# Kernel optimization log

Hardware: AMD Instinct MI355X
Metric: run time of the kernel (lower is better)

## Reference

```python
import jax, jax.numpy as jnp
import numpy as np

L = 3          # num_gc_layers
DIM = 128      # hidden dim (== num_features)
BN_EPS = 1e-5


def _bn(h, gamma, beta):
    # torch BatchNorm1d training-mode normalization (biased variance)
    m = h.mean(axis=0)
    v = h.var(axis=0)
    return gamma * (h - m) * jax.lax.rsqrt(v + BN_EPS) + beta


def setup_inputs() -> dict:
    key = jax.random.key(0)
    ks = jax.random.split(key, 24)
    N, E, G = 50000, 600000, 256
    s = 0.05
    inp = {
        "x": jax.random.normal(ks[0], (N, DIM), jnp.float32),
        "src": jax.random.randint(ks[1], (E,), 0, N, jnp.int32),
        "dst": jax.random.randint(ks[2], (E,), 0, N, jnp.int32),
        "batch": jnp.sort(jax.random.randint(ks[3], (N,), 0, G, jnp.int32)),
        "n_graphs": G,
        # GIN MLP params (stacked over layers; num_features == dim)
        "conv_w1": jax.random.normal(ks[4], (L, DIM, DIM), jnp.float32) * s,
        "conv_b1": jnp.zeros((L, DIM), jnp.float32),
        "conv_w2": jax.random.normal(ks[5], (L, DIM, DIM), jnp.float32) * s,
        "conv_b2": jnp.zeros((L, DIM), jnp.float32),
        "bn_gamma": jnp.ones((L, DIM), jnp.float32),
        "bn_beta": jnp.zeros((L, DIM), jnp.float32),
        # summary weighter (dim -> 1)
        "sw_w": jax.random.normal(ks[6], (DIM, 1), jnp.float32) * s,
        "sw_b": jnp.zeros((1,), jnp.float32),
        # VAE heads
        "nmu_w": jax.random.normal(ks[7], (DIM, DIM), jnp.float32) * s,
        "nmu_b": jnp.zeros((DIM,), jnp.float32),
        "nlv_w": jax.random.normal(ks[8], (DIM, DIM), jnp.float32) * s,
        "nlv_b": jnp.zeros((DIM,), jnp.float32),
        "gmu_w": jax.random.normal(ks[9], (DIM, DIM), jnp.float32) * s,
        "gmu_b": jnp.zeros((DIM,), jnp.float32),
        "glv_w": jax.random.normal(ks[10], (DIM, DIM), jnp.float32) * s,
        "glv_b": jnp.zeros((DIM,), jnp.float32),
        # head BN params, order: [node_mu, node_logvar, graph_mu, graph_logvar]
        "head_gamma": jnp.ones((4, DIM), jnp.float32),
        "head_beta": jnp.zeros((4, DIM), jnp.float32),
    }
    return inp


def reference(x, src, dst, batch, n_graphs,
              conv_w1, conv_b1, conv_w2, conv_b2, bn_gamma, bn_beta,
              sw_w, sw_b, nmu_w, nmu_b, nlv_w, nlv_b,
              gmu_w, gmu_b, glv_w, glv_b, head_gamma, head_beta):
    N = x.shape[0]
    for i in range(L):
        # GINConv (eps=0): h = nn(x + sum_{j->i} x_j)
        agg = jax.ops.segment_sum(x[src], dst, num_segments=N)  # [N, dim]
        h = x + agg
        h = jax.nn.relu(h @ conv_w1[i] + conv_b1[i]) @ conv_w2[i] + conv_b2[i]
        x = _bn(jax.nn.relu(h), bn_gamma[i], bn_beta[i])

    w = jax.nn.sigmoid(x @ sw_w + sw_b)           # [N, 1]
    summary_info = w * x                          # [N, dim]
    noisy_info = (1.0 - w) * x                    # [N, dim]
    slots = jax.ops.segment_sum(summary_info, batch, num_segments=n_graphs)  # [G, dim]

    node_mu = _bn(jax.nn.relu(noisy_info @ nmu_w + nmu_b), head_gamma[0], head_beta[0])
    node_logvar = _bn(jax.nn.relu(noisy_info @ nlv_w + nlv_b), head_gamma[1], head_beta[1])
    graph_mu = _bn(jax.nn.relu(slots @ gmu_w + gmu_b), head_gamma[2], head_beta[2])
    graph_logvar = _bn(jax.nn.relu(slots @ glv_w + glv_b), head_gamma[3], head_beta[3])
    return (node_mu, node_logvar, graph_mu, graph_logvar)
```

## Files before the change

kernel.cpp:

```cpp
#include <hip/hip_runtime.h>
#include <hip/hip_bf16.h>

#define DIM 128
#define BN_EPS 1e-5f
#define NSTRIPE 32

typedef unsigned short ushortT;
typedef __attribute__((ext_vector_type(8))) short short8;
typedef __attribute__((ext_vector_type(4))) float floatx4;

__device__ __forceinline__ float bflo(unsigned u) { return __uint_as_float(u << 16); }
__device__ __forceinline__ float bfhi(unsigned u) { return __uint_as_float(u & 0xffff0000u); }
__device__ __forceinline__ float bf2f(ushortT h) { return __uint_as_float(((unsigned)h) << 16); }
__device__ __forceinline__ ushortT f2bf(float f) {
    unsigned x = __float_as_uint(f);
    unsigned r = (x + 0x7fff + ((x >> 16) & 1)) >> 16;
    return (ushortT)r;
}
__device__ __forceinline__ void decode8(const unsigned* ap, short8& hi, short8& lo) {
#pragma unroll
    for (int j = 0; j < 8; ++j) {
        hi[j] = (short)(ap[j] >> 16);
        lo[j] = (short)(ap[j] & 0xffffu);
    }
}
__device__ __forceinline__ void acc8(float* a, uint4 v) {
    a[0] += bflo(v.x); a[1] += bfhi(v.x);
    a[2] += bflo(v.y); a[3] += bfhi(v.y);
    a[4] += bflo(v.z); a[5] += bfhi(v.z);
    a[6] += bflo(v.w); a[7] += bfhi(v.w);
}

__global__ __launch_bounds__(256) void hist_kernel(
    const int* __restrict__ dst, int* __restrict__ deg, int E)
{
    int e = blockIdx.x * 256 + threadIdx.x;
    if (e < E) atomicAdd(&deg[dst[e]], 1);
}

__global__ __launch_bounds__(256) void scan1_kernel(
    const int* __restrict__ deg, int* __restrict__ iscan,
    int* __restrict__ bsum, int N)
{
    __shared__ int s[256];
    int t = threadIdx.x;
    int i = blockIdx.x * 256 + t;
    int v = (i < N) ? deg[i] : 0;
    s[t] = v;
    __syncthreads();
#pragma unroll
    for (int off = 1; off < 256; off <<= 1) {
        int u = (t >= off) ? s[t - off] : 0;
        __syncthreads();
        s[t] += u;
        __syncthreads();
    }
    if (i < N) iscan[i] = s[t];
    if (t == 255) bsum[blockIdx.x] = s[255];
}

__global__ __launch_bounds__(256) void scan2_kernel(int* __restrict__ bsum, int nb)
{
    __shared__ int s[256];
    int t = threadIdx.x;
    int v = (t < nb) ? bsum[t] : 0;
    s[t] = v;
    __syncthreads();
#pragma unroll
    for (int off = 1; off < 256; off <<= 1) {
        int u = (t >= off) ? s[t - off] : 0;
        __syncthreads();
        s[t] += u;
        __syncthreads();
    }
    if (t < nb) bsum[t] = s[t] - v;
}

__global__ __launch_bounds__(256) void scan3_kernel(
    const int* __restrict__ iscan, const int* __restrict__ bsum,
    const int* __restrict__ deg, int* __restrict__ row_ptr,
    int* __restrict__ cur, int N)
{
    int i = blockIdx.x * 256 + threadIdx.x;
    if (i < N) {
        int inc = iscan[i] + bsum[i >> 8];
        row_ptr[i + 1] = inc;
        cur[i] = inc - deg[i];
    }
    if (i == 0) row_ptr[0] = 0;
}

__global__ __launch_bounds__(256) void fill_kernel(
    const int* __restrict__ src, const int* __restrict__ dst,
    int* __restrict__ cur, int* __restrict__ eidx, int E)
{
    int e = blockIdx.x * 256 + threadIdx.x;
    if (e < E) {
        int pos = atomicAdd(&cur[dst[e]], 1);
        eidx[pos] = src[e];
    }
}

__global__ __launch_bounds__(256) void convw_kernel(
    const float* __restrict__ cw1, const float* __restrict__ cw2,
    const float* __restrict__ nmu, const float* __restrict__ nlv,
    const float* __restrict__ gmu, const float* __restrict__ glv,
    ushortT* __restrict__ whi, ushortT* __restrict__ wlo)
{
    int tid = blockIdx.x * 256 + threadIdx.x;
    int mat = tid >> 14;
    int i   = tid & 16383;
    int n = i >> 7, k = i & 127;
    const float* Wm = (mat < 3) ? cw1 + (size_t)mat * 16384
                    : (mat < 6) ? cw2 + (size_t)(mat - 3) * 16384
                    : (mat == 6) ? nmu : (mat == 7) ? nlv
                    : (mat == 8) ? gmu : glv;
    float w = Wm[k * DIM + n];
    ushortT h = f2bf(w);
    whi[(size_t)mat * 16384 + i] = h;
    wlo[(size_t)mat * 16384 + i] = f2bf(w - bf2f(h));
}

__global__ __launch_bounds__(256) void convx_kernel(
    const float* __restrict__ x, ushortT* __restrict__ xb, int n8)
{
    int i = blockIdx.x * 256 + threadIdx.x;
    if (i >= n8) return;
    const float4* xp = (const float4*)x;
    float4 a = xp[2 * i], b = xp[2 * i + 1];
    uint4 o;
    o.x = (unsigned)f2bf(a.x) | ((unsigned)f2bf(a.y) << 16);
    o.y = (unsigned)f2bf(a.z) | ((unsigned)f2bf(a.w) << 16);
    o.z = (unsigned)f2bf(b.x) | ((unsigned)f2bf(b.y) << 16);
    o.w = (unsigned)f2bf(b.z) | ((unsigned)f2bf(b.w) << 16);
    ((uint4*)xb)[i] = o;
}

__global__ __launch_bounds__(256) void merge_stats_kernel(
    const float* __restrict__ sbuf, float* __restrict__ out)
{
    int t = threadIdx.x;
    float s = 0.f;
#pragma unroll
    for (int i = 0; i < NSTRIPE; ++i) s += sbuf[i * 256 + t];
    out[t] = s;
}

__global__ __launch_bounds__(256) void layer_fused_kernel(
    const ushortT* __restrict__ Xb, const int* __restrict__ row_ptr,
    const int* __restrict__ eidx,
    const float* __restrict__ ssum, const float* __restrict__ ssq,
    const float* __restrict__ gamma, const float* __restrict__ beta,
    const ushortT* __restrict__ W1hi, const ushortT* __restrict__ W1lo,
    const float* __restrict__ b1,
    const ushortT* __restrict__ W2hi, const ushortT* __restrict__ W2lo,
    const float* __restrict__ b2,
    ushortT* __restrict__ rout, float* __restrict__ sdst,
    int M, float invM)
{
    __shared__ unsigned As[32][DIM + 4];
    __shared__ float ls[DIM], lsq[DIM];
    int t = threadIdx.x;
    int wave = t >> 6, lane = t & 63, quad = lane >> 4, l16 = lane & 15;
    int m0 = blockIdx.x * 32;

    {
        int nloc = t >> 3;
        int c0   = (t & 7) * 16;
        int node = m0 + nloc;
        float acc[16];
#pragma unroll
        for (int j = 0; j < 16; ++j) acc[j] = 0.f;
        if (node < M) {
            int b = row_ptr[node];
            int e = row_ptr[node + 1];
            const ushortT* xrow = Xb + (size_t)node * DIM + c0;
            acc8(&acc[0], *(const uint4*)(xrow));
            acc8(&acc[8], *(const uint4*)(xrow + 8));
            int i = b;
            for (; i + 4 <= e; i += 4) {
                int s0 = eidx[i], s1 = eidx[i + 1], s2 = eidx[i + 2], s3 = eidx[i + 3];
                const ushortT* p0 = Xb + (size_t)s0 * DIM + c0;
                const ushortT* p1 = Xb + (size_t)s1 * DIM + c0;
                const ushortT* p2 = Xb + (size_t)s2 * DIM + c0;
                const ushortT* p3 = Xb + (size_t)s3 * DIM + c0;
                uint4 v00 = *(const uint4*)(p0), v01 = *(const uint4*)(p0 + 8);
                uint4 v10 = *(const uint4*)(p1), v11 = *(const uint4*)(p1 + 8);
                uint4 v20 = *(const uint4*)(p2), v21 = *(const uint4*)(p2 + 8);
                uint4 v30 = *(const uint4*)(p3), v31 = *(const uint4*)(p3 + 8);
                acc8(&acc[0], v00); acc8(&acc[8], v01);
                acc8(&acc[0], v10); acc8(&acc[8], v11);
                acc8(&acc[0], v20); acc8(&acc[8], v21);
                acc8(&acc[0], v30); acc8(&acc[8], v31);
            }
            for (; i < e; ++i) {
                const ushortT* sp = Xb + (size_t)eidx[i] * DIM + c0;
                acc8(&acc[0], *(const uint4*)(sp));
                acc8(&acc[8], *(const uint4*)(sp + 8));
            }
            if (ssum) {
                float cnt = (float)(e - b + 1);
#pragma unroll
                for (int jq = 0; jq < 4; ++jq) {
                    int c = c0 + jq * 4;
                    float4 sm = *(const float4*)(ssum + c);
                    float4 sq = *(const float4*)(ssq + c);
                    float4 gm = *(const float4*)(gamma + c);
                    float4 bt = *(const float4*)(beta + c);
                    float m, sc;
                    m = sm.x * invM; sc = gm.x * rsqrtf(sq.x * invM - m * m + BN_EPS);
                    acc[jq * 4 + 0] = sc * acc[jq * 4 + 0] + cnt * (bt.x - sc * m);
                    m = sm.y * invM; sc = gm.y * rsqrtf(sq.y * invM - m * m + BN_EPS);
                    acc[jq * 4 + 1] = sc * acc[jq * 4 + 1] + cnt * (bt.y - sc * m);
                    m = sm.z * invM; sc = gm.z * rsqrtf(sq.z * invM - m * m + BN_EPS);
                    acc[jq * 4 + 2] = sc * acc[jq * 4 + 2] + cnt * (bt.z - sc * m);
                    m = sm.w * invM; sc = gm.w * rsqrtf(sq.w * invM - m * m + BN_EPS);
                    acc[jq * 4 + 3] = sc * acc[jq * 4 + 3] + cnt * (bt.w - sc * m);
                }
            }
        }
        unsigned pk[16];
#pragma unroll
        for (int j = 0; j < 16; ++j) {
            ushortT h = f2bf(acc[j]);
            ushortT l = f2bf(acc[j] - bf2f(h));
            pk[j] = ((unsigned)h << 16) | l;
        }
#pragma unroll
        for (int j4 = 0; j4 < 4; ++j4)
            *(uint4*)&As[nloc][c0 + j4 * 4] = *(uint4*)&pk[j4 * 4];
    }
    if (t < DIM) { ls[t] = 0.f; lsq[t] = 0.f; }
    __syncthreads();

    int cbase = wave * 32;
    floatx4 acc[2][2];
#pragma unroll
    for (int mt = 0; mt < 2; ++mt)
#pragma unroll
        for (int nt = 0; nt < 2; ++nt)
            acc[mt][nt] = (floatx4){0.f, 0.f, 0.f, 0.f};

#pragma unroll
    for (int ks = 0; ks < 4; ++ks) {
        int k0 = ks * 32 + quad * 8;
        short8 bhi[2], blo[2];
#pragma unroll
        for (int nt = 0; nt < 2; ++nt) {
            const size_t woff = (size_t)(cbase + nt * 16 + l16) * DIM + k0;
            bhi[nt] = *(const short8*)(W1hi + woff);
            blo[nt] = *(const short8*)(W1lo + woff);
        }
#pragma unroll
        for (int mt = 0; mt < 2; ++mt) {
            int lr = mt * 16 + l16;
            unsigned ap[8];
            *(uint4*)&ap[0] = *(const uint4*)&As[lr][k0];
            *(uint4*)&ap[4] = *(const uint4*)&As[lr][k0 + 4];
            short8 ahi, alo;
            decode8(ap, ahi, alo);
#pragma unroll
            for (int nt = 0; nt < 2; ++nt) {
                acc[mt][nt] = __builtin_amdgcn_mfma_f32_16x16x32_bf16(ahi, bhi[nt], acc[mt][nt], 0, 0, 0);
                acc[mt][nt] = __builtin_amdgcn_mfma_f32_16x16x32_bf16(alo, bhi[nt], acc[mt][nt], 0, 0, 0);
                acc[mt][nt] = __builtin_amdgcn_mfma_f32_16x16x32_bf16(ahi, blo[nt], acc[mt][nt], 0, 0, 0);
            }
        }
    }
    __syncthreads();

#pragma unroll
    for (int nt = 0; nt < 2; ++nt) {
        int col = cbase + nt * 16 + l16;
        float bcol = b1[col];
#pragma unroll
        for (int mt = 0; mt < 2; ++mt)
#pragma unroll
            for (int r = 0; r < 4; ++r) {
                int lr = mt * 16 + quad * 4 + r;
                float v = fmaxf(acc[mt][nt][r] + bcol, 0.f);
                ushortT hv = f2bf(v);
                ushortT lv = f2bf(v - bf2f(hv));
                As[lr][col] = ((unsigned)hv << 16) | lv;
            }
    }
    __syncthreads();

#pragma unroll
    for (int mt = 0; mt < 2; ++mt)
#pragma unroll
        for (int nt = 0; nt < 2; ++nt)
            acc[mt][nt] = (floatx4){0.f, 0.f, 0.f, 0.f};

#pragma unroll
    for (int ks = 0; ks < 4; ++ks) {
        int k0 = ks * 32 + quad * 8;
        short8 bhi[2], blo[2];
#pragma unroll
        for (int nt = 0; nt < 2; ++nt) {
            const size_t woff = (size_t)(cbase + nt * 16 + l16) * DIM + k0;
            bhi[nt] = *(const short8*)(W2hi + woff);
            blo[nt] = *(const short8*)(W2lo + woff);
        }
#pragma unroll
        for (int mt = 0; mt < 2; ++mt) {
            int lr = mt * 16 + l16;
            unsigned ap[8];
            *(uint4*)&ap[0] = *(const uint4*)&As[lr][k0];
            *(uint4*)&ap[4] = *(const uint4*)&As[lr][k0 + 4];
            short8 ahi, alo;
            decode8(ap, ahi, alo);
#pragma unroll
            for (int nt = 0; nt < 2; ++nt) {
                acc[mt][nt] = __builtin_amdgcn_mfma_f32_16x16x32_bf16(ahi, bhi[nt], acc[mt][nt], 0, 0, 0);
                acc[mt][nt] = __builtin_amdgcn_mfma_f32_16x16x32_bf16(alo, bhi[nt], acc[mt][nt], 0, 0, 0);
                acc[mt][nt] = __builtin_amdgcn_mfma_f32_16x16x32_bf16(ahi, blo[nt], acc[mt][nt], 0, 0, 0);
            }
        }
    }
#pragma unroll
    for (int nt = 0; nt < 2; ++nt) {
        int col = cbase + nt * 16 + l16;
        float bcol = b2[col];
        float s = 0.f, sq = 0.f;
#pragma unroll
        for (int mt = 0; mt < 2; ++mt)
#pragma unroll
            for (int r = 0; r < 4; ++r) {
                int gr = m0 + mt * 16 + quad * 4 + r;
                if (gr < M) {
                    float v = fmaxf(acc[mt][nt][r] + bcol, 0.f);
                    rout[(size_t)gr * DIM + col] = f2bf(v);
                    s += v;
                    sq += v * v;
                }
            }
        s  += __shfl_xor(s, 16);  s  += __shfl_xor(s, 32);
        sq += __shfl_xor(sq, 16); sq += __shfl_xor(sq, 32);
        if (quad == 0) {
            atomicAdd(&ls[col], s);
            atomicAdd(&lsq[col], sq);
        }
    }
    __syncthreads();
    float* dstp = sdst + (size_t)(blockIdx.x & (NSTRIPE - 1)) * 256;
    if (t < 128) atomicAdd(&dstp[t], ls[t]);
    else         atomicAdd(&dstp[t], lsq[t - 128]);
}

__global__ __launch_bounds__(256) void heads_kernel(
    const unsigned* __restrict__ AP,
    const ushortT* __restrict__ WAhi, const ushortT* __restrict__ WAlo,
    const float* __restrict__ bA, ushortT* __restrict__ hA, float* __restrict__ sdstA,
    const ushortT* __restrict__ WBhi, const ushortT* __restrict__ WBlo,
    const float* __restrict__ bB, ushortT* __restrict__ hB, float* __restrict__ sdstB,
    int M)
{
    __shared__ float lsA[DIM], lsqA[DIM], lsB[DIM], lsqB[DIM];
    int t = threadIdx.x;
    int wave = t >> 6, lane = t & 63, quad = lane >> 4, l16 = lane & 15;
    int m0 = blockIdx.x * 64;
    int cbase = wave * 32;

    if (t < DIM) { lsA[t] = 0.f; lsqA[t] = 0.f; lsB[t] = 0.f; lsqB[t] = 0.f; }
    __syncthreads();

    floatx4 accA[4][2], accB[4][2];
#pragma unroll
    for (int mt = 0; mt < 4; ++mt)
#pragma unroll
        for (int nt = 0; nt < 2; ++nt) {
            accA[mt][nt] = (floatx4){0.f, 0.f, 0.f, 0.f};
            accB[mt][nt] = (floatx4){0.f, 0.f, 0.f, 0.f};
        }

    for (int ks = 0; ks < 4; ++ks) {
        int k0 = ks * 32 + quad * 8;
        short8 bAhi[2], bAlo[2], bBhi[2], bBlo[2];
#pragma unroll
        for (int nt = 0; nt < 2; ++nt) {
            const size_t woff = (size_t)(cbase + nt * 16 + l16) * DIM + k0;
            bAhi[nt] = *(const short8*)(WAhi + woff);
            bAlo[nt] = *(const short8*)(WAlo + woff);
            bBhi[nt] = *(const short8*)(WBhi + woff);
            bBlo[nt] = *(const short8*)(WBlo + woff);
        }
#pragma unroll
        for (int mt = 0; mt < 4; ++mt) {
            int row = m0 + mt * 16 + l16;
            unsigned ap[8] = {0, 0, 0, 0, 0, 0, 0, 0};
            if (row < M) {
                *(uint4*)&ap[0] = *(const uint4*)(AP + (size_t)row * DIM + k0);
                *(uint4*)&ap[4] = *(const uint4*)(AP + (size_t)row * DIM + k0 + 4);
            }
            short8 ahi, alo;
            decode8(ap, ahi, alo);
#pragma unroll
            for (int nt = 0; nt < 2; ++nt) {
                accA[mt][nt] = __builtin_amdgcn_mfma_f32_16x16x32_bf16(ahi, bAhi[nt], accA[mt][nt], 0, 0, 0);
                accA[mt][nt] = __builtin_amdgcn_mfma_f32_16x16x32_bf16(alo, bAhi[nt], accA[mt][nt], 0, 0, 0);
                accA[mt][nt] = __builtin_amdgcn_mfma_f32_16x16x32_bf16(ahi, bAlo[nt], accA[mt][nt], 0, 0, 0);
                accB[mt][nt] = __builtin_amdgcn_mfma_f32_16x16x32_bf16(ahi, bBhi[nt], accB[mt][nt], 0, 0, 0);
                accB[mt][nt] = __builtin_amdgcn_mfma_f32_16x16x32_bf16(alo, bBhi[nt], accB[mt][nt], 0, 0, 0);
                accB[mt][nt] = __builtin_amdgcn_mfma_f32_16x16x32_bf16(ahi, bBlo[nt], accB[mt][nt], 0, 0, 0);
            }
        }
    }

#pragma unroll
    for (int nt = 0; nt < 2; ++nt) {
        int col = cbase + nt * 16 + l16;
        float bcA = bA[col], bcB = bB[col];
        float sA = 0.f, sqA = 0.f, sB = 0.f, sqB = 0.f;
#pragma unroll
        for (int mt = 0; mt < 4; ++mt)
#pragma unroll
            for (int r = 0; r < 4; ++r) {
                int gr = m0 + mt * 16 + quad * 4 + r;
                if (gr < M) {
                    size_t off = (size_t)gr * DIM + col;
                    float vA = fmaxf(accA[mt][nt][r] + bcA, 0.f);
                    float vB = fmaxf(accB[mt][nt][r] + bcB, 0.f);
                    hA[off] = f2bf(vA);
                    hB[off] = f2bf(vB);
                    sA += vA; sqA += vA * vA;
                    sB += vB; sqB += vB * vB;
                }
            }
        sA += __shfl_xor(sA, 16);  sA += __shfl_xor(sA, 32);
        sqA += __shfl_xor(sqA, 16); sqA += __shfl_xor(sqA, 32);
        sB += __shfl_xor(sB, 16);  sB += __shfl_xor(sB, 32);
        sqB += __shfl_xor(sqB, 16); sqB += __shfl_xor(sqB, 32);
        if (quad == 0) {
            atomicAdd(&lsA[col], sA);
            atomicAdd(&lsqA[col], sqA);
            atomicAdd(&lsB[col], sB);
            atomicAdd(&lsqB[col], sqB);
        }
    }
    __syncthreads();
    int stripe = blockIdx.x & (NSTRIPE - 1);
    float* dA = sdstA + (size_t)stripe * 256;
    float* dB = sdstB + (size_t)stripe * 256;
    if (t < 128) { atomicAdd(&dA[t], lsA[t]); atomicAdd(&dB[t], lsB[t]); }
    else         { atomicAdd(&dA[t], lsqA[t - 128]); atomicAdd(&dB[t], lsqB[t - 128]); }
}

__global__ __launch_bounds__(256) void gemm_graph_kernel(
    const float* __restrict__ A32,
    const ushortT* __restrict__ Whi, const ushortT* __restrict__ Wlo,
    const float* __restrict__ bias, float* __restrict__ C,
    float* __restrict__ ssum, float* __restrict__ ssq, int M)
{
    __shared__ float ls[DIM], lsq[DIM];
    int t     = threadIdx.x;
    int wave  = t >> 6;
    int lane  = t & 63;
    int quad  = lane >> 4;
    int l16   = lane & 15;
    int m0    = blockIdx.x * 64;
    int cbase = wave * 32;

    if (t < DIM) { ls[t] = 0.f; lsq[t] = 0.f; }
    __syncthreads();

    floatx4 acc[4][2];
#pragma unroll
    for (int mt = 0; mt < 4; ++mt)
#pragma unroll
        for (int nt = 0; nt < 2; ++nt)
            acc[mt][nt] = (floatx4){0.f, 0.f, 0.f, 0.f};

    for (int ks = 0; ks < 4; ++ks) {
        int k0 = ks * 32 + quad * 8;
        short8 bhi[2], blo[2];
#pragma unroll
        for (int nt = 0; nt < 2; ++nt) {
            const size_t woff = (size_t)(cbase + nt * 16 + l16) * DIM + k0;
            bhi[nt] = *(const short8*)(Whi + woff);
            blo[nt] = *(const short8*)(Wlo + woff);
        }
#pragma unroll
        for (int mt = 0; mt < 4; ++mt) {
            int row = m0 + mt * 16 + l16;
            short8 ahi = {0,0,0,0,0,0,0,0};
            short8 alo = {0,0,0,0,0,0,0,0};
            if (row < M) {
                float av[8];
                *(float4*)&av[0] = *(const float4*)(A32 + (size_t)row * DIM + k0);
                *(float4*)&av[4] = *(const float4*)(A32 + (size_t)row * DIM + k0 + 4);
#pragma unroll
                for (int j = 0; j < 8; ++j) {
                    ushortT hv = f2bf(av[j]);
                    ahi[j] = (short)hv;
                    alo[j] = (short)f2bf(av[j] - bf2f(hv));
                }
            }
#pragma unroll
            for (int nt = 0; nt < 2; ++nt) {
                acc[mt][nt] = __builtin_amdgcn_mfma_f32_16x16x32_bf16(ahi, bhi[nt], acc[mt][nt], 0, 0, 0);
                acc[mt][nt] = __builtin_amdgcn_mfma_f32_16x16x32_bf16(alo, bhi[nt], acc[mt][nt], 0, 0, 0);
                acc[mt][nt] = __builtin_amdgcn_mfma_f32_16x16x32_bf16(ahi, blo[nt], acc[mt][nt], 0, 0, 0);
            }
        }
    }

#pragma unroll
    for (int nt = 0; nt < 2; ++nt) {
        int col = cbase + nt * 16 + l16;
        float bcol = bias[col];
        float s = 0.f, sq = 0.f;
#pragma unroll
        for (int mt = 0; mt < 4; ++mt)
#pragma unroll
            for (int r = 0; r < 4; ++r) {
                int gr = m0 + mt * 16 + quad * 4 + r;
                if (gr < M) {
                    float v = fmaxf(acc[mt][nt][r] + bcol, 0.f);
                    C[(size_t)gr * DIM + col] = v;
                    s += v;
                    sq += v * v;
                }
            }
        s  += __shfl_xor(s, 16);  s  += __shfl_xor(s, 32);
        sq += __shfl_xor(sq, 16); sq += __shfl_xor(sq, 32);
        if (quad == 0) {
            atomicAdd(&ls[col], s);
            atomicAdd(&lsq[col], sq);
        }
    }
    __syncthreads();
    if (t < DIM) {
        atomicAdd(&ssum[t], ls[t]);
        atomicAdd(&ssq[t], lsq[t]);
    }
}

__global__ __launch_bounds__(256) void bn_apply_kernel(
    const float* __restrict__ R, float* __restrict__ O,
    const float* __restrict__ sums, const float* __restrict__ sqsums,
    const float* __restrict__ gamma, const float* __restrict__ beta, int M)
{
    int idx = blockIdx.x * 256 + threadIdx.x;
    if (idx >= M * 32) return;
    int c4 = idx & 31;
    float invM = 1.0f / (float)M;
    float4 v = ((const float4*)R)[idx];
    float o[4] = {v.x, v.y, v.z, v.w};
#pragma unroll
    for (int j = 0; j < 4; ++j) {
        int c = c4 * 4 + j;
        float m   = sums[c] * invM;
        float var = sqsums[c] * invM - m * m;
        float sc  = gamma[c] * rsqrtf(var + BN_EPS);
        o[j] = sc * (o[j] - m) + beta[c];
    }
    ((float4*)O)[idx] = make_float4(o[0], o[1], o[2], o[3]);
}

__global__ __launch_bounds__(256) void bn_apply_bf16_kernel(
    const ushortT* __restrict__ R, float* __restrict__ O,
    const float* __restrict__ sums, const float* __restrict__ sqsums,
    const float* __restrict__ gamma, const float* __restrict__ beta, int M)
{
    int idx = blockIdx.x * 256 + threadIdx.x;
    if (idx >= M * 32) return;
    int c4 = idx & 31;
    float invM = 1.0f / (float)M;
    uint2 u = ((const uint2*)R)[idx];
    float o[4] = {bflo(u.x), bfhi(u.x), bflo(u.y), bfhi(u.y)};
#pragma unroll
    for (int j = 0; j < 4; ++j) {
        int c = c4 * 4 + j;
        float m   = sums[c] * invM;
        float var = sqsums[c] * invM - m * m;
        float sc  = gamma[c] * rsqrtf(var + BN_EPS);
        o[j] = sc * (o[j] - m) + beta[c];
    }
    ((float4*)O)[idx] = make_float4(o[0], o[1], o[2], o[3]);
}

__global__ __launch_bounds__(256) void weigh_split_kernel(
    const ushortT* __restrict__ R, const int* __restrict__ batch,
    const float* __restrict__ ssum, const float* __restrict__ ssq,
    const float* __restrict__ gamma, const float* __restrict__ beta,
    const float* __restrict__ sw_w, const float* __restrict__ sw_b,
    unsigned* __restrict__ noisyP, float* __restrict__ slots, int N, float invM)
{
    __shared__ float part[256];
    __shared__ float wsh[128];
    int t  = threadIdx.x;
    int r0 = blockIdx.x * 128;

    {
        int row  = r0 + (t >> 1);
        int cs   = (t & 1) * 64;
        float d = 0.f;
        if (row < N) {
            for (int c = cs; c < cs + 64; c += 4) {
                uint2 u = *(const uint2*)(R + (size_t)row * DIM + c);
                float rv[4] = {bflo(u.x), bfhi(u.x), bflo(u.y), bfhi(u.y)};
                float4 sm = *(const float4*)(ssum + c);
                float4 sq = *(const float4*)(ssq + c);
                float4 gm = *(const float4*)(gamma + c);
                float4 bt = *(const float4*)(beta + c);
                float4 sw = *(const float4*)(sw_w + c);
                float m, sc;
                m = sm.x * invM; sc = gm.x * rsqrtf(sq.x * invM - m * m + BN_EPS);
                d += (sc * (rv[0] - m) + bt.x) * sw.x;
                m = sm.y * invM; sc = gm.y * rsqrtf(sq.y * invM - m * m + BN_EPS);
                d += (sc * (rv[1] - m) + bt.y) * sw.y;
                m = sm.z * invM; sc = gm.z * rsqrtf(sq.z * invM - m * m + BN_EPS);
                d += (sc * (rv[2] - m) + bt.z) * sw.z;
                m = sm.w * invM; sc = gm.w * rsqrtf(sq.w * invM - m * m + BN_EPS);
                d += (sc * (rv[3] - m) + bt.w) * sw.w;
            }
        }
        part[t] = d;
    }
    __syncthreads();
    if (t < 128) {
        float dd = part[2 * t] + part[2 * t + 1];
        wsh[t] = 1.0f / (1.0f + expf(-(dd + sw_b[0])));
    }
    __syncthreads();

    int c    = t & 127;
    int half = t >> 7;
    int rend = r0 + 128;
    if (rend > N) rend = N;
    float m   = ssum[c] * invM;
    float var = ssq[c] * invM - m * m;
    float sc  = gamma[c] * rsqrtf(var + BN_EPS);
    float sh  = beta[c] - sc * m;
    int curg = -1;
    float acc = 0.f;
    for (int r = r0 + half; r < rend; r += 2) {
        float xv = sc * bf2f(R[(size_t)r * DIM + c]) + sh;
        float w  = wsh[r - r0];
        float nv = (1.f - w) * xv;
        ushortT hv = f2bf(nv);
        ushortT lv = f2bf(nv - bf2f(hv));
        noisyP[(size_t)r * DIM + c] = ((unsigned)hv << 16) | lv;
        int g = batch[r];
        if (g != curg) {
            if (curg >= 0) atomicAdd(&slots[(size_t)curg * DIM + c], acc);
            curg = g;
            acc = 0.f;
        }
        acc += w * xv;
    }
    if (curg >= 0) atomicAdd(&slots[(size_t)curg * DIM + c], acc);
}

extern "C" void kernel_launch(void* const* d_in, const int* in_sizes, int n_in,
                              void* d_out, int out_size, void* d_ws, size_t ws_size,
                              hipStream_t stream)
{
    const float* x      = (const float*)d_in[0];
    const int*   src    = (const int*)d_in[1];
    const int*   dst    = (const int*)d_in[2];
    const int*   batch  = (const int*)d_in[3];
    const float* cw1    = (const float*)d_in[5];
    const float* cb1    = (const float*)d_in[6];
    const float* cw2    = (const float*)d_in[7];
    const float* cb2    = (const float*)d_in[8];
    const float* bng    = (const float*)d_in[9];
    const float* bnb    = (const float*)d_in[10];
    const float* sw_w   = (const float*)d_in[11];
    const float* sw_b   = (const float*)d_in[12];
    const float* nmu_w  = (const float*)d_in[13];
    const float* nmu_b  = (const float*)d_in[14];
    const float* nlv_w  = (const float*)d_in[15];
    const float* nlv_b  = (const float*)d_in[16];
    const float* gmu_w  = (const float*)d_in[17];
    const float* gmu_b  = (const float*)d_in[18];
    const float* glv_w  = (const float*)d_in[19];
    const float* glv_b  = (const float*)d_in[20];
    const float* hgam   = (const float*)d_in[21];
    const float* hbet   = (const float*)d_in[22];

    const int N = in_sizes[0] / DIM;
    const int E = in_sizes[1];
    const int G = (out_size / DIM - 2 * N) / 2;

    float* out0 = (float*)d_out;
    float* out1 = out0 + (size_t)N * DIM;
    float* out2 = out1 + (size_t)N * DIM;
    float* out3 = out2 + (size_t)G * DIM;

    char* wp = (char*)d_ws;
    auto alloc = [&](size_t bytes) {
        char* p = wp;
        wp += (bytes + 255) & ~(size_t)255;
        return p;
    };
    ushortT*  xbf   = (ushortT*)alloc((size_t)N * DIM * 2);
    ushortT*  rA    = (ushortT*)alloc((size_t)N * DIM * 2);
    ushortT*  rB    = (ushortT*)alloc((size_t)N * DIM * 2);
    unsigned* noisyP= (unsigned*)alloc((size_t)N * DIM * 4);
    ushortT*  whi   = (ushortT*)alloc((size_t)10 * 16384 * 2);
    ushortT*  wlo   = (ushortT*)alloc((size_t)10 * 16384 * 2);
    float* slots    = (float*)alloc((size_t)G * DIM * 4);
    float* stats    = (float*)alloc((size_t)7 * 256 * 4);
    float* sbuf     = (float*)alloc((size_t)5 * NSTRIPE * 256 * 4);
    int* row_ptr    = (int*)alloc((size_t)(N + 2) * 4);
    int* eidx       = (int*)alloc((size_t)E * 4);
    int* deg   = (int*)noisyP;
    int* iscan = deg + N;
    int* bsum  = iscan + N;
    int* cur   = bsum + 256;

    auto SS = [&](int i) { return stats + (size_t)i * 256; };
    auto SQ = [&](int i) { return stats + (size_t)i * 256 + 128; };
    auto SB = [&](int i) { return sbuf + (size_t)i * NSTRIPE * 256; };

    const int edge_blocks  = (E + 255) / 256;
    const int scan_blocks  = (N + 255) / 256;
    const int layer_blocks = (N + 31) / 32;
    const int heads_blocks = (N + 63) / 64;
    const int g16_blocks   = (N * 16 + 255) / 256;
    const int g32_blocks   = (N * 32 + 255) / 256;
    const float invN = 1.0f / (float)N;

    hipMemsetAsync(stats, 0, (size_t)7 * 256 * 4, stream);
    hipMemsetAsync(sbuf, 0, (size_t)5 * NSTRIPE * 256 * 4, stream);
    hipMemsetAsync(slots, 0, (size_t)G * DIM * 4, stream);
    hipMemsetAsync(deg, 0, (size_t)N * 4, stream);

    convw_kernel<<<(10 * 16384) / 256, 256, 0, stream>>>(
        cw1, cw2, nmu_w, nlv_w, gmu_w, glv_w, whi, wlo);
    convx_kernel<<<g16_blocks, 256, 0, stream>>>(x, xbf, N * 16);

    hist_kernel<<<edge_blocks, 256, 0, stream>>>(dst, deg, E);
    scan1_kernel<<<scan_blocks, 256, 0, stream>>>(deg, iscan, bsum, N);
    scan2_kernel<<<1, 256, 0, stream>>>(bsum, scan_blocks);
    scan3_kernel<<<scan_blocks, 256, 0, stream>>>(iscan, bsum, deg, row_ptr, cur, N);
    fill_kernel<<<edge_blocks, 256, 0, stream>>>(src, dst, cur, eidx, E);

    const ushortT* lin[3]  = {xbf, rA, rB};
    ushortT*       lout[3] = {rA, rB, rA};
    for (int l = 0; l < 3; ++l) {
        const float* sums_prev = (l == 0) ? nullptr : SS(l - 1);
        const float* sq_prev   = (l == 0) ? nullptr : SQ(l - 1);
        const float* g_prev    = (l == 0) ? nullptr : bng + (size_t)(l - 1) * DIM;
        const float* b_prev    = (l == 0) ? nullptr : bnb + (size_t)(l - 1) * DIM;
        layer_fused_kernel<<<layer_blocks, 256, 0, stream>>>(
            lin[l], row_ptr, eidx,
            sums_prev, sq_prev, g_prev, b_prev,
            whi + (size_t)l * 16384, wlo + (size_t)l * 16384, cb1 + (size_t)l * DIM,
            whi + (size_t)(3 + l) * 16384, wlo + (size_t)(3 + l) * 16384, cb2 + (size_t)l * DIM,
            lout[l], SB(l), N, invN);
        merge_stats_kernel<<<1, 256, 0, stream>>>(SB(l), SS(l));
    }
    ushortT* rfin = rA;
    ushortT* hA   = rB;
    ushortT* hB   = xbf;

    weigh_split_kernel<<<(N + 127) / 128, 256, 0, stream>>>(
        rfin, batch, SS(2), SQ(2), bng + 2 * DIM, bnb + 2 * DIM,
        sw_w, sw_b, noisyP, slots, N, invN);

    heads_kernel<<<heads_blocks, 256, 0, stream>>>(
        noisyP,
        whi + (size_t)6 * 16384, wlo + (size_t)6 * 16384, nmu_b, hA, SB(3),
        whi + (size_t)7 * 16384, wlo + (size_t)7 * 16384, nlv_b, hB, SB(4), N);
    merge_stats_kernel<<<1, 256, 0, stream>>>(SB(3), SS(3));
    merge_stats_kernel<<<1, 256, 0, stream>>>(SB(4), SS(4));
    bn_apply_bf16_kernel<<<g32_blocks, 256, 0, stream>>>(
        hA, out0, SS(3), SQ(3), hgam + 0 * DIM, hbet + 0 * DIM, N);
    bn_apply_bf16_kernel<<<g32_blocks, 256, 0, stream>>>(
        hB, out1, SS(4), SQ(4), hgam + 1 * DIM, hbet + 1 * DIM, N);

    const int gemm_blocks_G = (G + 63) / 64;
    gemm_graph_kernel<<<gemm_blocks_G, 256, 0, stream>>>(
        slots, whi + (size_t)8 * 16384, wlo + (size_t)8 * 16384,
        gmu_b, out2, SS(5), SQ(5), G);
    gemm_graph_kernel<<<gemm_blocks_G, 256, 0, stream>>>(
        slots, whi + (size_t)9 * 16384, wlo + (size_t)9 * 16384,
        glv_b, out3, SS(6), SQ(6), G);
    bn_apply_kernel<<<(G * 32 + 255) / 256, 256, 0, stream>>>(
        out2, out2, SS(5), SQ(5), hgam + 2 * DIM, hbet + 2 * DIM, G);
    bn_apply_kernel<<<(G * 32 + 255) / 256, 256, 0, stream>>>(
        out3, out3, SS(6), SQ(6), hgam + 3 * DIM, hbet + 3 * DIM, G);
}
```

Measured before the change: 509.4 us.

## Merge small launches, fold stat merging into consumers, deepen gather unroll

Folds the weight conversion, input bf16 conversion and all memsets into a single prep kernel. Each layer kernel and the weigh-split kernel now reduces the striped statistics buffer itself instead of relying on separate merge launches. Paired head GEMM and BN-apply launches are combined into dual-dispatch kernels. The neighbour gather gains an 8-way unrolled loop, and the layer kernel gets a launch-bounds occupancy hint. The aim is to cut launch count and latency in exchange for redundant per-block stripe reduction work and higher register pressure.

```diff
diff --git a/kernel.cpp b/kernel.cpp
--- a/kernel.cpp
+++ b/kernel.cpp
@@ -101,55 +101,57 @@
     }
 }
 
-__global__ __launch_bounds__(256) void convw_kernel(
+__global__ __launch_bounds__(256) void prep_kernel(
     const float* __restrict__ cw1, const float* __restrict__ cw2,
     const float* __restrict__ nmu, const float* __restrict__ nlv,
     const float* __restrict__ gmu, const float* __restrict__ glv,
-    ushortT* __restrict__ whi, ushortT* __restrict__ wlo)
-{
-    int tid = blockIdx.x * 256 + threadIdx.x;
-    int mat = tid >> 14;
-    int i   = tid & 16383;
-    int n = i >> 7, k = i & 127;
-    const float* Wm = (mat < 3) ? cw1 + (size_t)mat * 16384
-                    : (mat < 6) ? cw2 + (size_t)(mat - 3) * 16384
-                    : (mat == 6) ? nmu : (mat == 7) ? nlv
-                    : (mat == 8) ? gmu : glv;
-    float w = Wm[k * DIM + n];
-    ushortT h = f2bf(w);
-    whi[(size_t)mat * 16384 + i] = h;
-    wlo[(size_t)mat * 16384 + i] = f2bf(w - bf2f(h));
-}
-
-__global__ __launch_bounds__(256) void convx_kernel(
-    const float* __restrict__ x, ushortT* __restrict__ xb, int n8)
-{
-    int i = blockIdx.x * 256 + threadIdx.x;
-    if (i >= n8) return;
-    const float4* xp = (const float4*)x;
-    float4 a = xp[2 * i], b = xp[2 * i + 1];
-    uint4 o;
-    o.x = (unsigned)f2bf(a.x) | ((unsigned)f2bf(a.y) << 16);
-    o.y = (unsigned)f2bf(a.z) | ((unsigned)f2bf(a.w) << 16);
-    o.z = (unsigned)f2bf(b.x) | ((unsigned)f2bf(b.y) << 16);
-    o.w = (unsigned)f2bf(b.z) | ((unsigned)f2bf(b.w) << 16);
-    ((uint4*)xb)[i] = o;
-}
-
-__global__ __launch_bounds__(256) void merge_stats_kernel(
-    const float* __restrict__ sbuf, float* __restrict__ out)
-{
-    int t = threadIdx.x;
-    float s = 0.f;
-#pragma unroll
-    for (int i = 0; i < NSTRIPE; ++i) s += sbuf[i * 256 + t];
-    out[t] = s;
-}
-
-__global__ __launch_bounds__(256) void layer_fused_kernel(
+    ushortT* __restrict__ whi, ushortT* __restrict__ wlo,
+    const float* __restrict__ x, ushortT* __restrict__ xb, int n8, int cxBlocks,
+    float4* __restrict__ zsbuf, int sbufQ,
+    float4* __restrict__ zslots, int slotsQ,
+    float4* __restrict__ zdeg, int degQ,
+    float4* __restrict__ zstats, int statsQ)
+{
+    int b = blockIdx.x, t = threadIdx.x;
+    if (b < 640) {
+        int tid = b * 256 + t;
+        int mat = tid >> 14;
+        int i   = tid & 16383;
+        int n = i >> 7, k = i & 127;
+        const float* Wm = (mat < 3) ? cw1 + (size_t)mat * 16384
+                        : (mat < 6) ? cw2 + (size_t)(mat - 3) * 16384
+                        : (mat == 6) ? nmu : (mat == 7) ? nlv
+                        : (mat == 8) ? gmu : glv;
+        float w = Wm[k * DIM + n];
+        ushortT h = f2bf(w);
+        whi[(size_t)mat * 16384 + i] = h;
+        wlo[(size_t)mat * 16384 + i] = f2bf(w - bf2f(h));
+    } else if (b < 640 + cxBlocks) {
+        int i = (b - 640) * 256 + t;
+        if (i < n8) {
+            const float4* xp = (const float4*)x;
+            float4 a = xp[2 * i], bb = xp[2 * i + 1];
+            uint4 o;
+            o.x = (unsigned)f2bf(a.x) | ((unsigned)f2bf(a.y) << 16);
+            o.y = (unsigned)f2bf(a.z) | ((unsigned)f2bf(a.w) << 16);
+            o.z = (unsigned)f2bf(bb.x) | ((unsigned)f2bf(bb.y) << 16);
+            o.w = (unsigned)f2bf(bb.z) | ((unsigned)f2bf(bb.w) << 16);
+            ((uint4*)xb)[i] = o;
+        }
+    } else {
+        int q = (b - 640 - cxBlocks) * 256 + t;
+        float4 z = make_float4(0.f, 0.f, 0.f, 0.f);
+        if (q < sbufQ) zsbuf[q] = z;
+        else if ((q -= sbufQ) < slotsQ) zslots[q] = z;
+        else if ((q -= slotsQ) < degQ) zdeg[q] = z;
+        else if ((q -= degQ) < statsQ) zstats[q] = z;
+    }
+}
+
+__global__ __launch_bounds__(256, 4) void layer_fused_kernel(
     const ushortT* __restrict__ Xb, const int* __restrict__ row_ptr,
     const int* __restrict__ eidx,
-    const float* __restrict__ ssum, const float* __restrict__ ssq,
+    const float* __restrict__ sprev,
     const float* __restrict__ gamma, const float* __restrict__ beta,
     const ushortT* __restrict__ W1hi, const ushortT* __restrict__ W1lo,
     const float* __restrict__ b1,
@@ -160,9 +162,19 @@
 {
     __shared__ unsigned As[32][DIM + 4];
     __shared__ float ls[DIM], lsq[DIM];
+    __shared__ float pstat[256];
     int t = threadIdx.x;
     int wave = t >> 6, lane = t & 63, quad = lane >> 4, l16 = lane & 15;
     int m0 = blockIdx.x * 32;
+
+    if (sprev) {
+        float s = 0.f;
+#pragma unroll
+        for (int i = 0; i < NSTRIPE; ++i) s += sprev[i * 256 + t];
+        pstat[t] = s;
+    }
+    if (t < DIM) { ls[t] = 0.f; lsq[t] = 0.f; }
+    __syncthreads();
 
     {
         int nloc = t >> 3;
@@ -178,6 +190,22 @@
             acc8(&acc[0], *(const uint4*)(xrow));
             acc8(&acc[8], *(const uint4*)(xrow + 8));
             int i = b;
+            for (; i + 8 <= e; i += 8) {
+                const ushortT* p[8];
+#pragma unroll
+                for (int j = 0; j < 8; ++j) p[j] = Xb + (size_t)eidx[i + j] * DIM + c0;
+                uint4 va[8], vb[8];
+#pragma unroll
+                for (int j = 0; j < 8; ++j) {
+                    va[j] = *(const uint4*)(p[j]);
+                    vb[j] = *(const uint4*)(p[j] + 8);
+                }
+#pragma unroll
+                for (int j = 0; j < 8; ++j) {
+                    acc8(&acc[0], va[j]);
+                    acc8(&acc[8], vb[j]);
+                }
+            }
             for (; i + 4 <= e; i += 4) {
                 int s0 = eidx[i], s1 = eidx[i + 1], s2 = eidx[i + 2], s3 = eidx[i + 3];
                 const ushortT* p0 = Xb + (size_t)s0 * DIM + c0;
@@ -198,13 +226,13 @@
                 acc8(&acc[0], *(const uint4*)(sp));
                 acc8(&acc[8], *(const uint4*)(sp + 8));
             }
-            if (ssum) {
+            if (sprev) {
                 float cnt = (float)(e - b + 1);
 #pragma unroll
                 for (int jq = 0; jq < 4; ++jq) {
                     int c = c0 + jq * 4;
-                    float4 sm = *(const float4*)(ssum + c);
-                    float4 sq = *(const float4*)(ssq + c);
+                    float4 sm = *(const float4*)&pstat[c];
+                    float4 sq = *(const float4*)&pstat[128 + c];
                     float4 gm = *(const float4*)(gamma + c);
                     float4 bt = *(const float4*)(beta + c);
                     float m, sc;
@@ -230,7 +258,6 @@
         for (int j4 = 0; j4 < 4; ++j4)
             *(uint4*)&As[nloc][c0 + j4 * 4] = *(uint4*)&pk[j4 * 4];
     }
-    if (t < DIM) { ls[t] = 0.f; lsq[t] = 0.f; }
     __syncthreads();
 
     int cbase = wave * 32;
@@ -446,19 +473,39 @@
     else         { atomicAdd(&dA[t], lsqA[t - 128]); atomicAdd(&dB[t], lsqB[t - 128]); }
 }
 
-__global__ __launch_bounds__(256) void gemm_graph_kernel(
+__global__ __launch_bounds__(256) void merge_stats2_kernel(
+    const float* __restrict__ sA, float* __restrict__ oA,
+    const float* __restrict__ sB, float* __restrict__ oB)
+{
+    const float* s = blockIdx.x ? sB : sA;
+    float* o = blockIdx.x ? oB : oA;
+    int t = threadIdx.x;
+    float v = 0.f;
+#pragma unroll
+    for (int i = 0; i < NSTRIPE; ++i) v += s[i * 256 + t];
+    o[t] = v;
+}
+
+__global__ __launch_bounds__(256) void gemm_graph_dual_kernel(
     const float* __restrict__ A32,
-    const ushortT* __restrict__ Whi, const ushortT* __restrict__ Wlo,
-    const float* __restrict__ bias, float* __restrict__ C,
-    float* __restrict__ ssum, float* __restrict__ ssq, int M)
+    const ushortT* __restrict__ W8hi, const ushortT* __restrict__ W8lo,
+    const float* __restrict__ b8, float* __restrict__ C8, float* __restrict__ st8,
+    const ushortT* __restrict__ W9hi, const ushortT* __restrict__ W9lo,
+    const float* __restrict__ b9, float* __restrict__ C9, float* __restrict__ st9,
+    int M, int nb)
 {
     __shared__ float ls[DIM], lsq[DIM];
+    int bb = blockIdx.x;
+    const ushortT* Whi; const ushortT* Wlo; const float* bias; float* C; float* st;
+    if (bb < nb) { Whi = W8hi; Wlo = W8lo; bias = b8; C = C8; st = st8; }
+    else { bb -= nb; Whi = W9hi; Wlo = W9lo; bias = b9; C = C9; st = st9; }
+
     int t     = threadIdx.x;
     int wave  = t >> 6;
     int lane  = t & 63;
     int quad  = lane >> 4;
     int l16   = lane & 15;
-    int m0    = blockIdx.x * 64;
+    int m0    = bb * 64;
     int cbase = wave * 32;
 
     if (t < DIM) { ls[t] = 0.f; lsq[t] = 0.f; }
@@ -531,39 +578,23 @@
     }
     __syncthreads();
     if (t < DIM) {
-        atomicAdd(&ssum[t], ls[t]);
-        atomicAdd(&ssq[t], lsq[t]);
-    }
-}
-
-__global__ __launch_bounds__(256) void bn_apply_kernel(
-    const float* __restrict__ R, float* __restrict__ O,
-    const float* __restrict__ sums, const float* __restrict__ sqsums,
-    const float* __restrict__ gamma, const float* __restrict__ beta, int M)
-{
-    int idx = blockIdx.x * 256 + threadIdx.x;
-    if (idx >= M * 32) return;
-    int c4 = idx & 31;
-    float invM = 1.0f / (float)M;
-    float4 v = ((const float4*)R)[idx];
-    float o[4] = {v.x, v.y, v.z, v.w};
-#pragma unroll
-    for (int j = 0; j < 4; ++j) {
-        int c = c4 * 4 + j;
-        float m   = sums[c] * invM;
-        float var = sqsums[c] * invM - m * m;
-        float sc  = gamma[c] * rsqrtf(var + BN_EPS);
-        o[j] = sc * (o[j] - m) + beta[c];
-    }
-    ((float4*)O)[idx] = make_float4(o[0], o[1], o[2], o[3]);
-}
-
-__global__ __launch_bounds__(256) void bn_apply_bf16_kernel(
-    const ushortT* __restrict__ R, float* __restrict__ O,
-    const float* __restrict__ sums, const float* __restrict__ sqsums,
-    const float* __restrict__ gamma, const float* __restrict__ beta, int M)
-{
-    int idx = blockIdx.x * 256 + threadIdx.x;
+        atomicAdd(&st[t], ls[t]);
+        atomicAdd(&st[DIM + t], lsq[t]);
+    }
+}
+
+__global__ __launch_bounds__(256) void bn_dual_bf16_kernel(
+    const ushortT* __restrict__ RA, float* __restrict__ OA, const float* __restrict__ stA,
+    const float* __restrict__ gA, const float* __restrict__ bA,
+    const ushortT* __restrict__ RB, float* __restrict__ OB, const float* __restrict__ stB,
+    const float* __restrict__ gB, const float* __restrict__ bB,
+    int M, int nb)
+{
+    int bb = blockIdx.x;
+    const ushortT* R; float* O; const float* st; const float* gamma; const float* beta;
+    if (bb < nb) { R = RA; O = OA; st = stA; gamma = gA; beta = bA; }
+    else { bb -= nb; R = RB; O = OB; st = stB; gamma = gB; beta = bB; }
+    int idx = bb * 256 + threadIdx.x;
     if (idx >= M * 32) return;
     int c4 = idx & 31;
     float invM = 1.0f / (float)M;
@@ -572,25 +603,62 @@
 #pragma unroll
     for (int j = 0; j < 4; ++j) {
         int c = c4 * 4 + j;
-        float m   = sums[c] * invM;
-        float var = sqsums[c] * invM - m * m;
+        float m   = st[c] * invM;
+        float var = st[DIM + c] * invM - m * m;
         float sc  = gamma[c] * rsqrtf(var + BN_EPS);
         o[j] = sc * (o[j] - m) + beta[c];
     }
     ((float4*)O)[idx] = make_float4(o[0], o[1], o[2], o[3]);
 }
 
+__global__ __launch_bounds__(256) void bn_dual_f32_kernel(
+    float* __restrict__ CA, const float* __restrict__ stA,
+    const float* __restrict__ gA, const float* __restrict__ bA,
+    float* __restrict__ CB, const float* __restrict__ stB,
+    const float* __restrict__ gB, const float* __restrict__ bB,
+    int M, int nb)
+{
+    int bb = blockIdx.x;
+    float* C; const float* st; const float* gamma; const float* beta;
+    if (bb < nb) { C = CA; st = stA; gamma = gA; beta = bA; }
+    else { bb -= nb; C = CB; st = stB; gamma = gB; beta = bB; }
+    int idx = bb * 256 + threadIdx.x;
+    if (idx >= M * 32) return;
+    int c4 = idx & 31;
+    float invM = 1.0f / (float)M;
+    float4 v = ((const float4*)C)[idx];
+    float o[4] = {v.x, v.y, v.z, v.w};
+#pragma unroll
+    for (int j = 0; j < 4; ++j) {
+        int c = c4 * 4 + j;
+        float m   = st[c] * invM;
+        float var = st[DIM + c] * invM - m * m;
+        float sc  = gamma[c] * rsqrtf(var + BN_EPS);
+        o[j] = sc * (o[j] - m) + beta[c];
+    }
+    ((float4*)C)[idx] = make_float4(o[0], o[1], o[2], o[3]);
+}
+
 __global__ __launch_bounds__(256) void weigh_split_kernel(
     const ushortT* __restrict__ R, const int* __restrict__ batch,
-    const float* __restrict__ ssum, const float* __restrict__ ssq,
+    const float* __restrict__ sprev,
     const float* __restrict__ gamma, const float* __restrict__ beta,
     const float* __restrict__ sw_w, const float* __restrict__ sw_b,
     unsigned* __restrict__ noisyP, float* __restrict__ slots, int N, float invM)
 {
     __shared__ float part[256];
     __shared__ float wsh[128];
+    __shared__ float pstat[256];
     int t  = threadIdx.x;
     int r0 = blockIdx.x * 128;
+
+    {
+        float s = 0.f;
+#pragma unroll
+        for (int i = 0; i < NSTRIPE; ++i) s += sprev[i * 256 + t];
+        pstat[t] = s;
+    }
+    __syncthreads();
 
     {
         int row  = r0 + (t >> 1);
@@ -600,8 +668,8 @@
             for (int c = cs; c < cs + 64; c += 4) {
                 uint2 u = *(const uint2*)(R + (size_t)row * DIM + c);
                 float rv[4] = {bflo(u.x), bfhi(u.x), bflo(u.y), bfhi(u.y)};
-                float4 sm = *(const float4*)(ssum + c);
-                float4 sq = *(const float4*)(ssq + c);
+                float4 sm = *(const float4*)&pstat[c];
+                float4 sq = *(const float4*)&pstat[128 + c];
                 float4 gm = *(const float4*)(gamma + c);
                 float4 bt = *(const float4*)(beta + c);
                 float4 sw = *(const float4*)(sw_w + c);
@@ -629,8 +697,8 @@
     int half = t >> 7;
     int rend = r0 + 128;
     if (rend > N) rend = N;
-    float m   = ssum[c] * invM;
-    float var = ssq[c] * invM - m * m;
+    float m   = pstat[c] * invM;
+    float var = pstat[128 + c] * invM - m * m;
     float sc  = gamma[c] * rsqrtf(var + BN_EPS);
     float sh  = beta[c] - sc * m;
     int curg = -1;
@@ -669,16 +737,16 @@
     const float* bnb    = (const float*)d_in[10];
     const float* sw_w   = (const float*)d_in[11];
     const float* sw_b   = (const float*)d_in[12];
-    const float* nmu_w  = (const float*)d_in[13];
     const float* nmu_b  = (const float*)d_in[14];
-    const float* nlv_w  = (const float*)d_in[15];
     const float* nlv_b  = (const float*)d_in[16];
-    const float* gmu_w  = (const float*)d_in[17];
     const float* gmu_b  = (const float*)d_in[18];
-    const float* glv_w  = (const float*)d_in[19];
     const float* glv_b  = (const float*)d_in[20];
     const float* hgam   = (const float*)d_in[21];
     const float* hbet   = (const float*)d_in[22];
+    const float* nmu_w  = (const float*)d_in[13];
+    const float* nlv_w  = (const float*)d_in[15];
+    const float* gmu_w  = (const float*)d_in[17];
+    const float* glv_w  = (const float*)d_in[19];
 
     const int N = in_sizes[0] / DIM;
     const int E = in_sizes[1];
@@ -712,7 +780,6 @@
     int* cur   = bsum + 256;
 
     auto SS = [&](int i) { return stats + (size_t)i * 256; };
-    auto SQ = [&](int i) { return stats + (size_t)i * 256 + 128; };
     auto SB = [&](int i) { return sbuf + (size_t)i * NSTRIPE * 256; };
 
     const int edge_blocks  = (E + 255) / 256;
@@ -723,14 +790,18 @@
     const int g32_blocks   = (N * 32 + 255) / 256;
     const float invN = 1.0f / (float)N;
 
-    hipMemsetAsync(stats, 0, (size_t)7 * 256 * 4, stream);
-    hipMemsetAsync(sbuf, 0, (size_t)5 * NSTRIPE * 256 * 4, stream);
-    hipMemsetAsync(slots, 0, (size_t)G * DIM * 4, stream);
-    hipMemsetAsync(deg, 0, (size_t)N * 4, stream);
-
-    convw_kernel<<<(10 * 16384) / 256, 256, 0, stream>>>(
-        cw1, cw2, nmu_w, nlv_w, gmu_w, glv_w, whi, wlo);
-    convx_kernel<<<g16_blocks, 256, 0, stream>>>(x, xbf, N * 16);
+    const int sbufQ  = (5 * NSTRIPE * 256) / 4;
+    const int slotsQ = (G * DIM) / 4;
+    const int degQ   = (N + 3) / 4;
+    const int statsQ = (7 * 256) / 4;
+    const int zeroQ  = sbufQ + slotsQ + degQ + statsQ;
+    const int zero_blocks = (zeroQ + 255) / 256;
+
+    prep_kernel<<<640 + g16_blocks + zero_blocks, 256, 0, stream>>>(
+        cw1, cw2, nmu_w, nlv_w, gmu_w, glv_w, whi, wlo,
+        x, xbf, N * 16, g16_blocks,
+        (float4*)sbuf, sbufQ, (float4*)slots, slotsQ,
+        (float4*)deg, degQ, (float4*)stats, statsQ);
 
     hist_kernel<<<edge_blocks, 256, 0, stream>>>(dst, deg, E);
     scan1_kernel<<<scan_blocks, 256, 0, stream>>>(deg, iscan, bsum, N);
@@ -741,46 +812,41 @@
     const ushortT* lin[3]  = {xbf, rA, rB};
     ushortT*       lout[3] = {rA, rB, rA};
     for (int l = 0; l < 3; ++l) {
-        const float* sums_prev = (l == 0) ? nullptr : SS(l - 1);
-        const float* sq_prev   = (l == 0) ? nullptr : SQ(l - 1);
-        const float* g_prev    = (l == 0) ? nullptr : bng + (size_t)(l - 1) * DIM;
-        const float* b_prev    = (l == 0) ? nullptr : bnb + (size_t)(l - 1) * DIM;
+        const float* sprev  = (l == 0) ? nullptr : SB(l - 1);
+        const float* g_prev = (l == 0) ? nullptr : bng + (size_t)(l - 1) * DIM;
+        const float* b_prev = (l == 0) ? nullptr : bnb + (size_t)(l - 1) * DIM;
         layer_fused_kernel<<<layer_blocks, 256, 0, stream>>>(
             lin[l], row_ptr, eidx,
-            sums_prev, sq_prev, g_prev, b_prev,
+            sprev, g_prev, b_prev,
             whi + (size_t)l * 16384, wlo + (size_t)l * 16384, cb1 + (size_t)l * DIM,
             whi + (size_t)(3 + l) * 16384, wlo + (size_t)(3 + l) * 16384, cb2 + (size_t)l * DIM,
             lout[l], SB(l), N, invN);
-        merge_stats_kernel<<<1, 256, 0, stream>>>(SB(l), SS(l));
     }
     ushortT* rfin = rA;
     ushortT* hA   = rB;
     ushortT* hB   = xbf;
 
     weigh_split_kernel<<<(N + 127) / 128, 256, 0, stream>>>(
-        rfin, batch, SS(2), SQ(2), bng + 2 * DIM, bnb + 2 * DIM,
+        rfin, batch, SB(2), bng + 2 * DIM, bnb + 2 * DIM,
         sw_w, sw_b, noisyP, slots, N, invN);
 
     heads_kernel<<<heads_blocks, 256, 0, stream>>>(
         noisyP,
         whi + (size_t)6 * 16384, wlo + (size_t)6 * 16384, nmu_b, hA, SB(3),
         whi + (size_t)7 * 16384, wlo + (size_t)7 * 16384, nlv_b, hB, SB(4), N);
-    merge_stats_kernel<<<1, 256, 0, stream>>>(SB(3), SS(3));
-    merge_stats_kernel<<<1, 256, 0, stream>>>(SB(4), SS(4));
-    bn_apply_bf16_kernel<<<g32_blocks, 256, 0, stream>>>(
-        hA, out0, SS(3), SQ(3), hgam + 0 * DIM, hbet + 0 * DIM, N);
-    bn_apply_bf16_kernel<<<g32_blocks, 256, 0, stream>>>(
-        hB, out1, SS(4), SQ(4), hgam + 1 * DIM, hbet + 1 * DIM, N);
+    merge_stats2_kernel<<<2, 256, 0, stream>>>(SB(3), SS(3), SB(4), SS(4));
+    bn_dual_bf16_kernel<<<2 * g32_blocks, 256, 0, stream>>>(
+        hA, out0, SS(3), hgam + 0 * DIM, hbet + 0 * DIM,
+        hB, out1, SS(4), hgam + 1 * DIM, hbet + 1 * DIM, N, g32_blocks);
 
     const int gemm_blocks_G = (G + 63) / 64;
-    gemm_graph_kernel<<<gemm_blocks_G, 256, 0, stream>>>(
-        slots, whi + (size_t)8 * 16384, wlo + (size_t)8 * 16384,
-        gmu_b, out2, SS(5), SQ(5), G);
-    gemm_graph_kernel<<<gemm_blocks_G, 256, 0, stream>>>(
-        slots, whi + (size_t)9 * 16384, wlo + (size_t)9 * 16384,
-        glv_b, out3, SS(6), SQ(6), G);
-    bn_apply_kernel<<<(G * 32 + 255) / 256, 256, 0, stream>>>(
-        out2, out2, SS(5), SQ(5), hgam + 2 * DIM, hbet + 2 * DIM, G);
-    bn_apply_kernel<<<(G * 32 + 255) / 256, 256, 0, stream>>>(
-        out3, out3, SS(6), SQ(6), hgam + 3 * DIM, hbet + 3 * DIM, G);
-}
+    const int gbn_blocks    = (G * 32 + 255) / 256;
+    gemm_graph_dual_kernel<<<2 * gemm_blocks_G, 256, 0, stream>>>(
+        slots,
+        whi + (size_t)8 * 16384, wlo + (size_t)8 * 16384, gmu_b, out2, SS(5),
+        whi + (size_t)9 * 16384, wlo + (size_t)9 * 16384, glv_b, out3, SS(6),
+        G, gemm_blocks_G);
+    bn_dual_f32_kernel<<<2 * gbn_blocks, 256, 0, stream>>>(
+        out2, SS(5), hgam + 2 * DIM, hbet + 2 * DIM,
+        out3, SS(6), hgam + 3 * DIM, hbet + 3 * DIM, G, gbn_blocks);
+}
```

Result: slower. 531.9 us (+4.4%).
